# Kernel optimization log

Measured on AMD Instinct MI355X. Metric: run time of the kernel, lower is better.

Reference implementation:

```python
import jax, jax.numpy as jnp
import numpy as np
from jax import lax

M, N, Q = 256, 65536, 64
LAMBDA_STAR = 0.1
LAMBDA_O = 0.1
T_ITERS = 16
PM_ITERS = 100


def setup_inputs() -> dict:
    key = jax.random.key(0)
    kx, kd = jax.random.split(key)
    X = jax.random.normal(kx, (M, N), dtype=jnp.float32)
    D = jax.random.normal(kd, (M, Q), dtype=jnp.float32)
    return {"X": X, "D": D}


def _power_method(D):
    # Largest eigenvalue of D^T D via 100-step power iteration (fixed random init).
    x0 = jax.random.normal(jax.random.key(1), (1, Q), dtype=D.dtype)

    def step(x, _):
        x = (x @ D.T) @ D          # [1,q] -> [1,m] -> [1,q]
        nm = jnp.linalg.norm(x)
        return x / nm, nm

    _, nms = lax.scan(step, x0, None, length=PM_ITERS)
    return nms[-1]


def reference(X, D):
    m, n = X.shape
    q = D.shape[1]
    alpha = _power_method(D)
    eta = 1.0 / alpha

    Iq = jnp.eye(q, dtype=D.dtype)
    Im = jnp.eye(m, dtype=D.dtype)
    top = jnp.concatenate([D.T @ D + LAMBDA_STAR * Iq, D.T], axis=1)   # [q, q+m]
    bot = jnp.concatenate([D, (1.0 + LAMBDA_STAR) * Im], axis=1)       # [m, q+m]
    H = jnp.eye(m + q, dtype=D.dtype) - eta * jnp.concatenate([top, bot], axis=0)
    W = eta * jnp.concatenate([D.T, Im], axis=0)                        # [(m+q), m]
    t = LAMBDA_O * eta * jnp.concatenate([jnp.zeros(q, D.dtype), jnp.ones(m, D.dtype)])

    b0 = W @ X                                                           # [(m+q), n]
    Z0 = jnp.zeros((m + q, n), dtype=X.dtype)

    def ista_step(carry, _):
        Z, b = carry
        Znew = jnp.maximum(0.0, b - t[:, None])    # thresholding (ger(t, ones) == t broadcast)
        b = b + H @ (Znew - Z)
        return (Znew, b), None

    (Z, _), _ = lax.scan(ista_step, (Z0, b0), None, length=T_ITERS)
    return Z
```

## Files before the change

kernel.cpp:

```cpp
#include <hip/hip_runtime.h>


typedef __bf16 bf16x8 __attribute__((ext_vector_type(8)));
typedef __bf16 bf16x2 __attribute__((ext_vector_type(2)));
typedef float f32x4 __attribute__((ext_vector_type(4)));
typedef float f32x2 __attribute__((ext_vector_type(2)));

#define MFMA16(a, b, c) __builtin_amdgcn_mfma_f32_16x16x32_bf16((a), (b), (c), 0, 0, 0)

#define NTOT 65536
#define NCOL 32

__device__ __forceinline__ unsigned pk2(float a, float b) {
#if __has_builtin(__builtin_amdgcn_cvt_pk_bf16_f32)
  return __builtin_bit_cast(unsigned, __builtin_amdgcn_cvt_pk_bf16_f32(a, b));
#else
  unsigned short ua = __builtin_bit_cast(unsigned short, (__bf16)a);
  unsigned short ub = __builtin_bit_cast(unsigned short, (__bf16)b);
  return (unsigned)ua | ((unsigned)ub << 16);
#endif
}
__device__ __forceinline__ unsigned pk2v(f32x2 v) { return pk2(v[0], v[1]); }
__device__ __forceinline__ f32x2 f2(float s) { f32x2 v = {s, s}; return v; }
__device__ __forceinline__ f32x2 pfma(f32x2 a, f32x2 b, f32x2 c) {
  return __builtin_elementwise_fma(a, b, c);
}
__device__ __forceinline__ f32x2 pmax0(f32x2 a) {
  return __builtin_elementwise_max(a, f2(0.f));
}

#define GOF(row) ((row) * 68 + (((row) >> 3) << 2))
__global__ void rnmf_prep(const float* __restrict__ D, void* __restrict__ ws) {
  float* wsf = (float*)ws;
  __bf16* Dbf = (__bf16*)((char*)ws + 256);
  __bf16* DTbf = (__bf16*)((char*)ws + 256 + 32768);

  __shared__ __bf16 DTl[64 * 264];
  __shared__ __bf16 gA[64 * 72];
  __shared__ __bf16 gB[64 * 72];
  __shared__ float gf[64 * 68 + 32];
  __shared__ __align__(16) float xv[64];

  const int tid = threadIdx.x;
  const int w = tid >> 6, lane = tid & 63, c = lane & 15, q4 = lane >> 4;

#pragma unroll
  for (int e = 0; e < 16; ++e) {
    int i4 = e * 256 + tid;
    float4 dv = *(const float4*)(D + i4 * 4);
    uint2 u; u.x = pk2(dv.x, dv.y); u.y = pk2(dv.z, dv.w);
    *(uint2*)(Dbf + i4 * 4) = u;
  }
#pragma unroll
  for (int e = 0; e < 64; ++e) {
    int flat = e * 256 + tid;
    int k = flat >> 6, a = flat & 63;
    DTl[a * 264 + k] = (__bf16)D[k * 64 + a];
  }
  __syncthreads();
#pragma unroll
  for (int e = 0; e < 8; ++e) {
    int fi = e * 256 + tid;
    int a = fi >> 5;
    int k = (fi * 8) & 255;
    *(bf16x8*)(DTbf + fi * 8) = *(const bf16x8*)&DTl[a * 264 + k];
  }
#pragma unroll
  for (int ct = 0; ct < 4; ++ct) {
    f32x4 acc = {0.f, 0.f, 0.f, 0.f};
#pragma unroll
    for (int kb = 0; kb < 8; ++kb) {
      bf16x8 a = *(const bf16x8*)&DTl[(16 * w + c) * 264 + 32 * kb + 8 * q4];
      bf16x8 b = *(const bf16x8*)&DTl[(16 * ct + c) * 264 + 32 * kb + 8 * q4];
      acc = MFMA16(a, b, acc);
    }
#pragma unroll
    for (int r = 0; r < 4; ++r)
      gA[(16 * w + 4 * q4 + r) * 72 + 16 * ct + c] = (__bf16)acc[r];
  }
  __syncthreads();
#pragma unroll
  for (int ct = 0; ct < 4; ++ct) {
    f32x4 acc = {0.f, 0.f, 0.f, 0.f};
#pragma unroll
    for (int kb = 0; kb < 2; ++kb) {
      bf16x8 a = *(const bf16x8*)&gA[(16 * w + c) * 72 + 32 * kb + 8 * q4];
      bf16x8 b = *(const bf16x8*)&gA[(16 * ct + c) * 72 + 32 * kb + 8 * q4];
      acc = MFMA16(a, b, acc);
    }
#pragma unroll
    for (int r = 0; r < 4; ++r)
      gB[(16 * w + 4 * q4 + r) * 72 + 16 * ct + c] = (__bf16)acc[r];
  }
  __syncthreads();
#pragma unroll
  for (int ct = 0; ct < 4; ++ct) {
    f32x4 acc = {0.f, 0.f, 0.f, 0.f};
#pragma unroll
    for (int kb = 0; kb < 2; ++kb) {
      bf16x8 a = *(const bf16x8*)&gB[(16 * w + c) * 72 + 32 * kb + 8 * q4];
      bf16x8 b = *(const bf16x8*)&gB[(16 * ct + c) * 72 + 32 * kb + 8 * q4];
      acc = MFMA16(a, b, acc);
    }
#pragma unroll
    for (int r = 0; r < 4; ++r)
      gA[(16 * w + 4 * q4 + r) * 72 + 16 * ct + c] = (__bf16)acc[r];
  }
  __syncthreads();
#pragma unroll
  for (int ct = 0; ct < 4; ++ct) {
    f32x4 acc = {0.f, 0.f, 0.f, 0.f};
#pragma unroll
    for (int kb = 0; kb < 2; ++kb) {
      bf16x8 a = *(const bf16x8*)&gA[(16 * w + c) * 72 + 32 * kb + 8 * q4];
      bf16x8 b = *(const bf16x8*)&gA[(16 * ct + c) * 72 + 32 * kb + 8 * q4];
      acc = MFMA16(a, b, acc);
    }
#pragma unroll
    for (int r = 0; r < 4; ++r)
      gf[GOF(16 * w + 4 * q4 + r) + 16 * ct + c] = acc[r];
  }
  __syncthreads();

  if (w == 0) {
    float td = gf[GOF(lane) + lane];
#pragma unroll
    for (int off = 32; off; off >>= 1) td += __shfl_xor(td, off, 64);
    const float tr = td;
    const float itr = 1.f / tr;
    xv[lane] = 1.f;
    float nm = 1.f;
    const int rowoff = GOF(lane);
    for (int itp = 0; itp < 28; ++itp) {
      float acc = 0.f;
#pragma unroll
      for (int k = 0; k < 64; k += 4) {
        float4 g = *(const float4*)&gf[rowoff + k];
        float4 xx = *(const float4*)&xv[k];
        acc = fmaf(g.x, xx.x, acc);
        acc = fmaf(g.y, xx.y, acc);
        acc = fmaf(g.z, xx.z, acc);
        acc = fmaf(g.w, xx.w, acc);
      }
      float y = acc * itr;
      float n2 = y * y;
#pragma unroll
      for (int off = 32; off; off >>= 1) n2 += __shfl_xor(n2, off, 64);
      nm = sqrtf(n2);
      xv[lane] = y / nm;
    }
    if (lane == 0) wsf[0] = 1.f / powf(nm * tr, 0.125f);
  }
}

__global__ __launch_bounds__(256, 3) void rnmf_main(const float* __restrict__ X,
                                                    float* __restrict__ Z,
                                                    const void* __restrict__ ws) {
  const float* wsf = (const float*)ws;
  const __bf16* Dbf = (const __bf16*)((const char*)ws + 256);
  const __bf16* DTbf = (const __bf16*)((const char*)ws + 256 + 32768);

  __shared__ __align__(16) char arena[33280];
  float* xs = (float*)arena;

  const int tid = threadIdx.x;
  const int w = tid >> 6;
  const int lane = tid & 63;
  const int c = lane & 15;
  const int q4 = lane >> 4;
  const int q4h = q4 >> 1, q4l = q4 & 1;
  const int j0 = blockIdx.x * NCOL;

#pragma unroll
  for (int e = 0; e < 8; ++e) {
    int idx = e * 256 + tid;
    int row = idx >> 3, c4 = (idx & 7) * 4;
    float4 g = *(const float4*)(X + row * NTOT + j0 + c4);
    xs[(c4 + 0) * 260 + row] = g.x;
    xs[(c4 + 1) * 260 + row] = g.y;
    xs[(c4 + 2) * 260 + row] = g.z;
    xs[(c4 + 3) * 260 + row] = g.w;
  }

  const float eta = wsf[0];
  const f32x2 etav = f2(eta);
  const f32x2 metav = f2(-eta);
  const f32x2 cqv = f2(1.f - 0.1f * eta);
  const f32x2 cmv = f2(1.f - 1.1f * eta);
  const float tm = 0.1f * eta;

  bf16x8 d1[4][2];
#pragma unroll
  for (int rt = 0; rt < 4; ++rt)
#pragma unroll
    for (int kb = 0; kb < 2; ++kb)
      d1[rt][kb] = *(const bf16x8*)(Dbf + (64 * w + 16 * rt + c) * 64 + 32 * kb + 8 * q4);
  bf16x8 d2[8];
#pragma unroll
  for (int kb = 0; kb < 8; ++kb)
    d2[kb] = *(const bf16x8*)(DTbf + (16 * w + c) * 256 + 32 * kb + 8 * q4);

  __syncthreads();

  f32x2 bqt2[2][2];
#pragma unroll
  for (int ct = 0; ct < 2; ++ct) {
    f32x4 acc = {0.f, 0.f, 0.f, 0.f};
#pragma unroll
    for (int kb = 0; kb < 8; ++kb) {
      const float* p = &xs[(16 * ct + c) * 260 + 32 * kb + 8 * q4];
      float4 lo = *(const float4*)p;
      float4 hi = *(const float4*)(p + 4);
      unsigned p0 = pk2(lo.x, lo.y), p1 = pk2(lo.z, lo.w);
      unsigned p2 = pk2(hi.x, hi.y), p3 = pk2(hi.z, hi.w);
      uint4 packed = {p0, p1, p2, p3};
      acc = MFMA16(d2[kb], __builtin_bit_cast(bf16x8, packed), acc);
    }
    f32x2 a0 = {acc[0], acc[1]}, a1 = {acc[2], acc[3]};
    bqt2[ct][0] = etav * a0;
    bqt2[ct][1] = etav * a1;
  }

  f32x2 bmt2[4][2][2];
#pragma unroll
  for (int rt = 0; rt < 4; ++rt)
#pragma unroll
    for (int ct = 0; ct < 2; ++ct) {
      const float* p = &xs[(16 * ct + c) * 260 + 64 * w + 16 * rt + 4 * q4];
      float4 v = *(const float4*)p;
      f32x2 x0 = {v.x, v.y}, x1 = {v.z, v.w};
      bmt2[rt][ct][0] = pfma(etav, x0, f2(-tm));
      bmt2[rt][ct][1] = pfma(etav, x1, f2(-tm));
    }

  __syncthreads();

  f32x2 zq2[2][2], zm2[4][2][2];
#pragma unroll
  for (int ct = 0; ct < 2; ++ct)
#pragma unroll
    for (int p = 0; p < 2; ++p) zq2[ct][p] = pmax0(bqt2[ct][p]);
#pragma unroll
  for (int rt = 0; rt < 4; ++rt)
#pragma unroll
    for (int ct = 0; ct < 2; ++ct)
#pragma unroll
      for (int p = 0; p < 2; ++p) zm2[rt][ct][p] = pmax0(bmt2[rt][ct][p]);

  char* smem = arena;
  const int rb = lane * 16;
  const int wzq = (w >> 1) * 1024 + ((2 * w) & 3) * 256 + q4h * 256 + c * 16 + 8 * q4l;
  const int wvb = 4096 + 2 * w * 1024 + q4h * 256 + c * 16 + 8 * q4l;

#pragma unroll
  for (int ct = 0; ct < 2; ++ct) {
    uint2 u; u.x = pk2v(zq2[ct][0]); u.y = pk2v(zq2[ct][1]);
    *(uint2*)(smem + wzq + ct * 2048) = u;
  }

  for (int it = 0; it < 15; ++it) {
    __syncthreads();
#pragma unroll
    for (int ct = 0; ct < 2; ++ct) {
      bf16x8 bz0 = *(const bf16x8*)(smem + rb + ct * 2048);
      bf16x8 bz1 = *(const bf16x8*)(smem + rb + ct * 2048 + 1024);
#pragma unroll
      for (int rt = 0; rt < 4; ++rt) {
        f32x4 acc = {0.f, 0.f, 0.f, 0.f};
        acc = MFMA16(d1[rt][0], bz0, acc);
        acc = MFMA16(d1[rt][1], bz1, acc);
        f32x2 u0 = {acc[0], acc[1]}, u1 = {acc[2], acc[3]};
        f32x2 z0 = zm2[rt][ct][0], z1 = zm2[rt][ct][1];
        f32x2 v0 = u0 + z0, v1 = u1 + z1;
        f32x2 t0 = pfma(cmv, z0, bmt2[rt][ct][0]);
        f32x2 t1 = pfma(cmv, z1, bmt2[rt][ct][1]);
        zm2[rt][ct][0] = pmax0(pfma(metav, u0, t0));
        zm2[rt][ct][1] = pmax0(pfma(metav, u1, t1));
        uint2 uu; uu.x = pk2v(v0); uu.y = pk2v(v1);
        *(uint2*)(smem + wvb + ct * 8192 + rt * 512) = uu;
      }
    }
    __syncthreads();
#pragma unroll
    for (int ct = 0; ct < 2; ++ct) {
      f32x4 acc = {0.f, 0.f, 0.f, 0.f};
#pragma unroll
      for (int kb = 0; kb < 8; ++kb) {
        bf16x8 bv = *(const bf16x8*)(smem + rb + 4096 + ct * 8192 + kb * 1024);
        acc = MFMA16(d2[kb], bv, acc);
      }
      f32x2 w0 = {acc[0], acc[1]}, w1 = {acc[2], acc[3]};
      f32x2 t0 = pfma(cqv, zq2[ct][0], bqt2[ct][0]);
      f32x2 t1 = pfma(cqv, zq2[ct][1], bqt2[ct][1]);
      zq2[ct][0] = pmax0(pfma(metav, w0, t0));
      zq2[ct][1] = pmax0(pfma(metav, w1, t1));
      uint2 u; u.x = pk2v(zq2[ct][0]); u.y = pk2v(zq2[ct][1]);
      *(uint2*)(smem + wzq + ct * 2048) = u;
    }
  }

#pragma unroll
  for (int ct = 0; ct < 2; ++ct)
#pragma unroll
    for (int p = 0; p < 2; ++p)
#pragma unroll
      for (int e = 0; e < 2; ++e)
        Z[(16 * w + 4 * q4 + 2 * p + e) * NTOT + j0 + 16 * ct + c] = zq2[ct][p][e];
#pragma unroll
  for (int rt = 0; rt < 4; ++rt)
#pragma unroll
    for (int ct = 0; ct < 2; ++ct)
#pragma unroll
      for (int p = 0; p < 2; ++p)
#pragma unroll
        for (int e = 0; e < 2; ++e)
          Z[(64 + 64 * w + 16 * rt + 4 * q4 + 2 * p + e) * NTOT + j0 + 16 * ct + c] = zm2[rt][ct][p][e];
}

extern "C" void kernel_launch(void* const* d_in, const int* in_sizes, int n_in,
                              void* d_out, int out_size, void* d_ws, size_t ws_size,
                              hipStream_t stream) {
  const float* X = (const float*)d_in[0];
  const float* D = (const float*)d_in[1];
  float* Z = (float*)d_out;
  rnmf_prep<<<dim3(1), dim3(256), 0, stream>>>(D, d_ws);
  rnmf_main<<<dim3(NTOT / NCOL), dim3(256), 0, stream>>>(X, Z, d_ws);
}
```

Baseline: 229.4 us.

## Split main-kernel waves 2x2 over rows and columns, reuse packed X and split MFMA chains

The main kernel's four waves are remapped from a row-only split over both 16-column tiles to a 2x2 grid: each wave now owns half the rows and a single column tile. D fragments held in registers double (d1 8x2, d2 2x8), the bf16-packed X operand is built once and reused across both Q row tiles, and the D^T·V accumulation runs as two independent MFMA chains summed at the end, exposing more MFMA parallelism. Launch bounds drop from 3 to 2 blocks per CU to fit the extra registers, which reduces occupancy. The prep kernel's power-iteration dot product is also split into four accumulators to shorten its dependency chain.

```diff
diff --git a/kernel.cpp b/kernel.cpp
--- a/kernel.cpp
+++ b/kernel.cpp
@@ -132,16 +132,27 @@
     float nm = 1.f;
     const int rowoff = GOF(lane);
     for (int itp = 0; itp < 28; ++itp) {
-      float acc = 0.f;
-#pragma unroll
-      for (int k = 0; k < 64; k += 4) {
-        float4 g = *(const float4*)&gf[rowoff + k];
-        float4 xx = *(const float4*)&xv[k];
-        acc = fmaf(g.x, xx.x, acc);
-        acc = fmaf(g.y, xx.y, acc);
-        acc = fmaf(g.z, xx.z, acc);
-        acc = fmaf(g.w, xx.w, acc);
+      float a0 = 0.f, a1 = 0.f, a2 = 0.f, a3 = 0.f;
+#pragma unroll
+      for (int k = 0; k < 64; k += 16) {
+        float4 ga = *(const float4*)&gf[rowoff + k];
+        float4 xa = *(const float4*)&xv[k];
+        float4 gb = *(const float4*)&gf[rowoff + k + 4];
+        float4 xb = *(const float4*)&xv[k + 4];
+        float4 gc = *(const float4*)&gf[rowoff + k + 8];
+        float4 xc = *(const float4*)&xv[k + 8];
+        float4 gd = *(const float4*)&gf[rowoff + k + 12];
+        float4 xd = *(const float4*)&xv[k + 12];
+        a0 = fmaf(ga.x, xa.x, a0); a0 = fmaf(ga.y, xa.y, a0);
+        a0 = fmaf(ga.z, xa.z, a0); a0 = fmaf(ga.w, xa.w, a0);
+        a1 = fmaf(gb.x, xb.x, a1); a1 = fmaf(gb.y, xb.y, a1);
+        a1 = fmaf(gb.z, xb.z, a1); a1 = fmaf(gb.w, xb.w, a1);
+        a2 = fmaf(gc.x, xc.x, a2); a2 = fmaf(gc.y, xc.y, a2);
+        a2 = fmaf(gc.z, xc.z, a2); a2 = fmaf(gc.w, xc.w, a2);
+        a3 = fmaf(gd.x, xd.x, a3); a3 = fmaf(gd.y, xd.y, a3);
+        a3 = fmaf(gd.z, xd.z, a3); a3 = fmaf(gd.w, xd.w, a3);
       }
+      float acc = (a0 + a1) + (a2 + a3);
       float y = acc * itr;
       float n2 = y * y;
 #pragma unroll
@@ -153,7 +164,7 @@
   }
 }
 
-__global__ __launch_bounds__(256, 3) void rnmf_main(const float* __restrict__ X,
+__global__ __launch_bounds__(256, 2) void rnmf_main(const float* __restrict__ X,
                                                     float* __restrict__ Z,
                                                     const void* __restrict__ ws) {
   const float* wsf = (const float*)ws;
@@ -169,6 +180,7 @@
   const int c = lane & 15;
   const int q4 = lane >> 4;
   const int q4h = q4 >> 1, q4l = q4 & 1;
+  const int wr = w >> 1, wc = w & 1;
   const int j0 = blockIdx.x * NCOL;
 
 #pragma unroll
@@ -189,132 +201,147 @@
   const f32x2 cmv = f2(1.f - 1.1f * eta);
   const float tm = 0.1f * eta;
 
-  bf16x8 d1[4][2];
-#pragma unroll
-  for (int rt = 0; rt < 4; ++rt)
+  bf16x8 d1[8][2];
+#pragma unroll
+  for (int rt = 0; rt < 8; ++rt)
 #pragma unroll
     for (int kb = 0; kb < 2; ++kb)
-      d1[rt][kb] = *(const bf16x8*)(Dbf + (64 * w + 16 * rt + c) * 64 + 32 * kb + 8 * q4);
-  bf16x8 d2[8];
-#pragma unroll
-  for (int kb = 0; kb < 8; ++kb)
-    d2[kb] = *(const bf16x8*)(DTbf + (16 * w + c) * 256 + 32 * kb + 8 * q4);
-
-  __syncthreads();
+      d1[rt][kb] = *(const bf16x8*)(Dbf + (128 * wr + 16 * rt + c) * 64 + 32 * kb + 8 * q4);
+  bf16x8 d2[2][8];
+#pragma unroll
+  for (int rt2 = 0; rt2 < 2; ++rt2)
+#pragma unroll
+    for (int kb = 0; kb < 8; ++kb)
+      d2[rt2][kb] = *(const bf16x8*)(DTbf + (32 * wr + 16 * rt2 + c) * 256 + 32 * kb + 8 * q4);
+
+  __syncthreads();
+
+  bf16x8 xb[8];
+#pragma unroll
+  for (int kb = 0; kb < 8; ++kb) {
+    const float* p = &xs[(16 * wc + c) * 260 + 32 * kb + 8 * q4];
+    float4 lo = *(const float4*)p;
+    float4 hi = *(const float4*)(p + 4);
+    uint4 packed = {pk2(lo.x, lo.y), pk2(lo.z, lo.w), pk2(hi.x, hi.y), pk2(hi.z, hi.w)};
+    xb[kb] = __builtin_bit_cast(bf16x8, packed);
+  }
 
   f32x2 bqt2[2][2];
 #pragma unroll
-  for (int ct = 0; ct < 2; ++ct) {
-    f32x4 acc = {0.f, 0.f, 0.f, 0.f};
-#pragma unroll
-    for (int kb = 0; kb < 8; ++kb) {
-      const float* p = &xs[(16 * ct + c) * 260 + 32 * kb + 8 * q4];
-      float4 lo = *(const float4*)p;
-      float4 hi = *(const float4*)(p + 4);
-      unsigned p0 = pk2(lo.x, lo.y), p1 = pk2(lo.z, lo.w);
-      unsigned p2 = pk2(hi.x, hi.y), p3 = pk2(hi.z, hi.w);
-      uint4 packed = {p0, p1, p2, p3};
-      acc = MFMA16(d2[kb], __builtin_bit_cast(bf16x8, packed), acc);
-    }
+  for (int rt2 = 0; rt2 < 2; ++rt2) {
+    f32x4 acc = {0.f, 0.f, 0.f, 0.f};
+#pragma unroll
+    for (int kb = 0; kb < 8; ++kb) acc = MFMA16(d2[rt2][kb], xb[kb], acc);
     f32x2 a0 = {acc[0], acc[1]}, a1 = {acc[2], acc[3]};
-    bqt2[ct][0] = etav * a0;
-    bqt2[ct][1] = etav * a1;
-  }
-
-  f32x2 bmt2[4][2][2];
-#pragma unroll
-  for (int rt = 0; rt < 4; ++rt)
-#pragma unroll
-    for (int ct = 0; ct < 2; ++ct) {
-      const float* p = &xs[(16 * ct + c) * 260 + 64 * w + 16 * rt + 4 * q4];
-      float4 v = *(const float4*)p;
-      f32x2 x0 = {v.x, v.y}, x1 = {v.z, v.w};
-      bmt2[rt][ct][0] = pfma(etav, x0, f2(-tm));
-      bmt2[rt][ct][1] = pfma(etav, x1, f2(-tm));
-    }
-
-  __syncthreads();
-
-  f32x2 zq2[2][2], zm2[4][2][2];
-#pragma unroll
-  for (int ct = 0; ct < 2; ++ct)
-#pragma unroll
-    for (int p = 0; p < 2; ++p) zq2[ct][p] = pmax0(bqt2[ct][p]);
-#pragma unroll
-  for (int rt = 0; rt < 4; ++rt)
-#pragma unroll
-    for (int ct = 0; ct < 2; ++ct)
-#pragma unroll
-      for (int p = 0; p < 2; ++p) zm2[rt][ct][p] = pmax0(bmt2[rt][ct][p]);
+    bqt2[rt2][0] = etav * a0;
+    bqt2[rt2][1] = etav * a1;
+  }
+
+  f32x2 bmt2[8][2];
+#pragma unroll
+  for (int rt = 0; rt < 8; ++rt) {
+    const float* p = &xs[(16 * wc + c) * 260 + 128 * wr + 16 * rt + 4 * q4];
+    float4 v = *(const float4*)p;
+    f32x2 x0 = {v.x, v.y}, x1 = {v.z, v.w};
+    bmt2[rt][0] = pfma(etav, x0, f2(-tm));
+    bmt2[rt][1] = pfma(etav, x1, f2(-tm));
+  }
+
+  __syncthreads();
+
+  f32x2 zq2[2][2], zm2[8][2];
+#pragma unroll
+  for (int rt2 = 0; rt2 < 2; ++rt2)
+#pragma unroll
+    for (int p = 0; p < 2; ++p) zq2[rt2][p] = pmax0(bqt2[rt2][p]);
+#pragma unroll
+  for (int rt = 0; rt < 8; ++rt)
+#pragma unroll
+    for (int p = 0; p < 2; ++p) zm2[rt][p] = pmax0(bmt2[rt][p]);
 
   char* smem = arena;
   const int rb = lane * 16;
-  const int wzq = (w >> 1) * 1024 + ((2 * w) & 3) * 256 + q4h * 256 + c * 16 + 8 * q4l;
-  const int wvb = 4096 + 2 * w * 1024 + q4h * 256 + c * 16 + 8 * q4l;
-
-#pragma unroll
-  for (int ct = 0; ct < 2; ++ct) {
-    uint2 u; u.x = pk2v(zq2[ct][0]); u.y = pk2v(zq2[ct][1]);
-    *(uint2*)(smem + wzq + ct * 2048) = u;
+  const int zqrd = wc * 2048 + rb;
+  const int vrd = 4096 + wc * 8192 + rb;
+  const int wzq = wc * 2048 + wr * 1024 + q4h * 256 + c * 16 + 8 * q4l;
+  const int wvb = 4096 + wc * 8192 + wr * 4096 + q4h * 256 + c * 16 + 8 * q4l;
+
+#pragma unroll
+  for (int rt2 = 0; rt2 < 2; ++rt2) {
+    uint2 u; u.x = pk2v(zq2[rt2][0]); u.y = pk2v(zq2[rt2][1]);
+    *(uint2*)(smem + wzq + rt2 * 512) = u;
   }
 
   for (int it = 0; it < 15; ++it) {
     __syncthreads();
-#pragma unroll
-    for (int ct = 0; ct < 2; ++ct) {
-      bf16x8 bz0 = *(const bf16x8*)(smem + rb + ct * 2048);
-      bf16x8 bz1 = *(const bf16x8*)(smem + rb + ct * 2048 + 1024);
-#pragma unroll
-      for (int rt = 0; rt < 4; ++rt) {
-        f32x4 acc = {0.f, 0.f, 0.f, 0.f};
-        acc = MFMA16(d1[rt][0], bz0, acc);
-        acc = MFMA16(d1[rt][1], bz1, acc);
-        f32x2 u0 = {acc[0], acc[1]}, u1 = {acc[2], acc[3]};
-        f32x2 z0 = zm2[rt][ct][0], z1 = zm2[rt][ct][1];
-        f32x2 v0 = u0 + z0, v1 = u1 + z1;
-        f32x2 t0 = pfma(cmv, z0, bmt2[rt][ct][0]);
-        f32x2 t1 = pfma(cmv, z1, bmt2[rt][ct][1]);
-        zm2[rt][ct][0] = pmax0(pfma(metav, u0, t0));
-        zm2[rt][ct][1] = pmax0(pfma(metav, u1, t1));
-        uint2 uu; uu.x = pk2v(v0); uu.y = pk2v(v1);
-        *(uint2*)(smem + wvb + ct * 8192 + rt * 512) = uu;
-      }
+    bf16x8 bz0 = *(const bf16x8*)(smem + zqrd);
+    bf16x8 bz1 = *(const bf16x8*)(smem + zqrd + 1024);
+#pragma unroll
+    for (int rt = 0; rt < 8; ++rt) {
+      f32x4 acc = {0.f, 0.f, 0.f, 0.f};
+      acc = MFMA16(d1[rt][0], bz0, acc);
+      acc = MFMA16(d1[rt][1], bz1, acc);
+      f32x2 u0 = {acc[0], acc[1]}, u1 = {acc[2], acc[3]};
+      f32x2 z0 = zm2[rt][0], z1v = zm2[rt][1];
+      f32x2 v0 = u0 + z0, v1 = u1 + z1v;
+      f32x2 t0 = pfma(cmv, z0, bmt2[rt][0]);
+      f32x2 t1 = pfma(cmv, z1v, bmt2[rt][1]);
+      zm2[rt][0] = pmax0(pfma(metav, u0, t0));
+      zm2[rt][1] = pmax0(pfma(metav, u1, t1));
+      uint2 uu; uu.x = pk2v(v0); uu.y = pk2v(v1);
+      *(uint2*)(smem + wvb + rt * 512) = uu;
     }
     __syncthreads();
-#pragma unroll
-    for (int ct = 0; ct < 2; ++ct) {
-      f32x4 acc = {0.f, 0.f, 0.f, 0.f};
-#pragma unroll
-      for (int kb = 0; kb < 8; ++kb) {
-        bf16x8 bv = *(const bf16x8*)(smem + rb + 4096 + ct * 8192 + kb * 1024);
-        acc = MFMA16(d2[kb], bv, acc);
-      }
-      f32x2 w0 = {acc[0], acc[1]}, w1 = {acc[2], acc[3]};
-      f32x2 t0 = pfma(cqv, zq2[ct][0], bqt2[ct][0]);
-      f32x2 t1 = pfma(cqv, zq2[ct][1], bqt2[ct][1]);
-      zq2[ct][0] = pmax0(pfma(metav, w0, t0));
-      zq2[ct][1] = pmax0(pfma(metav, w1, t1));
-      uint2 u; u.x = pk2v(zq2[ct][0]); u.y = pk2v(zq2[ct][1]);
-      *(uint2*)(smem + wzq + ct * 2048) = u;
-    }
-  }
-
-#pragma unroll
-  for (int ct = 0; ct < 2; ++ct)
+    f32x4 aA0 = {0.f, 0.f, 0.f, 0.f}, aA1 = {0.f, 0.f, 0.f, 0.f};
+    f32x4 aB0 = {0.f, 0.f, 0.f, 0.f}, aB1 = {0.f, 0.f, 0.f, 0.f};
+#pragma unroll
+    for (int kb = 0; kb < 4; ++kb) {
+      bf16x8 bv = *(const bf16x8*)(smem + vrd + kb * 1024);
+      aA0 = MFMA16(d2[0][kb], bv, aA0);
+      aA1 = MFMA16(d2[1][kb], bv, aA1);
+    }
+#pragma unroll
+    for (int kb = 4; kb < 8; ++kb) {
+      bf16x8 bv = *(const bf16x8*)(smem + vrd + kb * 1024);
+      aB0 = MFMA16(d2[0][kb], bv, aB0);
+      aB1 = MFMA16(d2[1][kb], bv, aB1);
+    }
+    f32x4 s0 = aA0 + aB0;
+    f32x4 s1 = aA1 + aB1;
+    {
+      f32x2 w0 = {s0[0], s0[1]}, w1 = {s0[2], s0[3]};
+      f32x2 t0 = pfma(cqv, zq2[0][0], bqt2[0][0]);
+      f32x2 t1 = pfma(cqv, zq2[0][1], bqt2[0][1]);
+      zq2[0][0] = pmax0(pfma(metav, w0, t0));
+      zq2[0][1] = pmax0(pfma(metav, w1, t1));
+      uint2 u; u.x = pk2v(zq2[0][0]); u.y = pk2v(zq2[0][1]);
+      *(uint2*)(smem + wzq) = u;
+    }
+    {
+      f32x2 w0 = {s1[0], s1[1]}, w1 = {s1[2], s1[3]};
+      f32x2 t0 = pfma(cqv, zq2[1][0], bqt2[1][0]);
+      f32x2 t1 = pfma(cqv, zq2[1][1], bqt2[1][1]);
+      zq2[1][0] = pmax0(pfma(metav, w0, t0));
+      zq2[1][1] = pmax0(pfma(metav, w1, t1));
+      uint2 u; u.x = pk2v(zq2[1][0]); u.y = pk2v(zq2[1][1]);
+      *(uint2*)(smem + wzq + 512) = u;
+    }
+  }
+
+#pragma unroll
+  for (int rt2 = 0; rt2 < 2; ++rt2)
 #pragma unroll
     for (int p = 0; p < 2; ++p)
 #pragma unroll
       for (int e = 0; e < 2; ++e)
-        Z[(16 * w + 4 * q4 + 2 * p + e) * NTOT + j0 + 16 * ct + c] = zq2[ct][p][e];
-#pragma unroll
-  for (int rt = 0; rt < 4; ++rt)
-#pragma unroll
-    for (int ct = 0; ct < 2; ++ct)
-#pragma unroll
-      for (int p = 0; p < 2; ++p)
-#pragma unroll
-        for (int e = 0; e < 2; ++e)
-          Z[(64 + 64 * w + 16 * rt + 4 * q4 + 2 * p + e) * NTOT + j0 + 16 * ct + c] = zm2[rt][ct][p][e];
+        Z[(32 * wr + 16 * rt2 + 4 * q4 + 2 * p + e) * NTOT + j0 + 16 * wc + c] = zq2[rt2][p][e];
+#pragma unroll
+  for (int rt = 0; rt < 8; ++rt)
+#pragma unroll
+    for (int p = 0; p < 2; ++p)
+#pragma unroll
+      for (int e = 0; e < 2; ++e)
+        Z[(64 + 128 * wr + 16 * rt + 4 * q4 + 2 * p + e) * NTOT + j0 + 16 * wc + c] = zm2[rt][p][e];
 }
 
 extern "C" void kernel_launch(void* const* d_in, const int* in_sizes, int n_in,
```

New measurement: 224.7 us. -2.1%, faster.
